# Kernel optimization log

Measured on AMD Instinct MI355X. Metric: run time of the kernel, lower is better.

## Reference

```python
import jax, jax.numpy as jnp
import numpy as np
from jax import lax

D_MODEL = 1024
D_STATE = 16
D_CONV = 4
EXPAND = 2
D_INNER = EXPAND * D_MODEL  # 2048
DT_RANK = (D_MODEL + 15) // 16  # 64 (ceil(d_model/16), mamba default)
BATCH = 2
SEQLEN = 1024


def setup_inputs() -> dict:
    key = jax.random.key(0)
    ks = jax.random.split(key, 12)
    s = lambda k, shape, sc=0.02: jax.random.normal(k, shape, jnp.float32) * sc
    # A init: S4D-real, A_log = log(1..d_state) tiled over channels
    A_log = jnp.log(jnp.tile(jnp.arange(1, D_STATE + 1, dtype=jnp.float32), (D_INNER, 1)))
    # dt bias init so softplus(dt_bias) ~ 0.01
    dt_bias = jnp.log(jnp.expm1(jnp.full((D_INNER,), 0.01, jnp.float32)))
    return {
        "x": jax.random.normal(ks[0], (BATCH, SEQLEN, D_MODEL), jnp.float32),
        "in_proj_w": s(ks[1], (2 * D_INNER, D_MODEL)),
        "conv_w": s(ks[2], (D_INNER, 1, D_CONV), 0.1),
        "conv_b": s(ks[3], (D_INNER,), 0.1),
        "x_proj_w": s(ks[4], (DT_RANK + 2 * D_STATE, D_INNER)),
        "dt_proj_w": s(ks[5], (D_INNER, DT_RANK), 0.1),
        "dt_proj_b": dt_bias,
        "A_log": A_log,
        "D": jnp.ones((D_INNER,), jnp.float32),
        "out_proj_w": s(ks[6], (D_MODEL, D_INNER)),
        "ln1_g": jnp.ones((D_MODEL,), jnp.float32),
        "ln1_b": jnp.zeros((D_MODEL,), jnp.float32),
        "ln2_g": jnp.ones((D_MODEL,), jnp.float32),
        "ln2_b": jnp.zeros((D_MODEL,), jnp.float32),
        "ffn_w1": s(ks[7], (4 * D_MODEL, D_MODEL)),
        "ffn_b1": jnp.zeros((4 * D_MODEL,), jnp.float32),
        "ffn_w2": s(ks[8], (D_MODEL, 4 * D_MODEL)),
        "ffn_b2": jnp.zeros((D_MODEL,), jnp.float32),
    }


def _layernorm(x, g, b, eps=1e-5):
    mu = jnp.mean(x, axis=-1, keepdims=True)
    var = jnp.mean(jnp.square(x - mu), axis=-1, keepdims=True)
    return (x - mu) * lax.rsqrt(var + eps) * g + b


def _mamba(x, in_proj_w, conv_w, conv_b, x_proj_w, dt_proj_w, dt_proj_b,
           A_log, D, out_proj_w):
    Bsz, L, _ = x.shape
    xz = x @ in_proj_w.T                       # [B, L, 2*d_inner]
    xi, z = jnp.split(xz, 2, axis=-1)          # each [B, L, d_inner]
    # causal depthwise conv1d over time
    xc = xi.transpose(0, 2, 1)                 # [B, d_inner, L]
    xc = lax.conv_general_dilated(
        xc, conv_w, window_strides=(1,), padding=[(D_CONV - 1, 0)],
        feature_group_count=D_INNER,
        dimension_numbers=("NCH", "OIH", "NCH"))
    xc = xc + conv_b[None, :, None]
    xc = jax.nn.silu(xc).transpose(0, 2, 1)    # [B, L, d_inner]
    # input-dependent SSM params
    x_dbl = xc @ x_proj_w.T                    # [B, L, dt_rank + 2*d_state]
    dt, Bmat, Cmat = jnp.split(x_dbl, [DT_RANK, DT_RANK + D_STATE], axis=-1)
    dt = jax.nn.softplus(dt @ dt_proj_w.T + dt_proj_b)   # [B, L, d_inner]
    A = -jnp.exp(A_log)                        # [d_inner, d_state]
    dA = jnp.exp(dt[..., None] * A)                       # [B, L, d_inner, d_state]
    dBx = dt[..., None] * Bmat[:, :, None, :] * xc[..., None]  # [B, L, d_inner, d_state]
    # selective scan over time
    def step(h, inp):
        dA_t, dBx_t, C_t = inp
        h = dA_t * h + dBx_t                   # [B, d_inner, d_state]
        y = jnp.einsum("bdn,bn->bd", h, C_t)
        return h, y
    h0 = jnp.zeros((Bsz, D_INNER, D_STATE), x.dtype)
    _, ys = lax.scan(step, h0,
                     (dA.transpose(1, 0, 2, 3),
                      dBx.transpose(1, 0, 2, 3),
                      Cmat.transpose(1, 0, 2)))
    y = ys.transpose(1, 0, 2)                  # [B, L, d_inner]
    y = y + D * xc
    y = y * jax.nn.silu(z)
    return y @ out_proj_w.T                    # [B, L, d_model]


def reference(x, in_proj_w, conv_w, conv_b, x_proj_w, dt_proj_w, dt_proj_b,
              A_log, D, out_proj_w, ln1_g, ln1_b, ln2_g, ln2_b,
              ffn_w1, ffn_b1, ffn_w2, ffn_b2):
    # x = x + Mamba(LN1(x))
    x = x + _mamba(_layernorm(x, ln1_g, ln1_b), in_proj_w, conv_w, conv_b,
                   x_proj_w, dt_proj_w, dt_proj_b, A_log, D, out_proj_w)
    # x = x + FFN(LN2(x))  (dropout inactive in eval)
    h = _layernorm(x, ln2_g, ln2_b)
    f = jax.nn.relu(h @ ffn_w1.T + ffn_b1) @ ffn_w2.T + ffn_b2
    return x + f
```

## Files before the change

kernel.cpp:

```cpp
#include <hip/hip_runtime.h>
#include <hip/hip_bf16.h>

#define T_TOK 2048
#define LSEQ  1024
#define DM    1024
#define DI    2048
#define LDW2  72

using bf16 = __hip_bfloat16;
typedef __attribute__((ext_vector_type(8))) short short8;
typedef __attribute__((ext_vector_type(4))) short short4b;
typedef __attribute__((ext_vector_type(4))) float floatx4;

__device__ inline float to_f(float v) { return v; }
__device__ inline float to_f(bf16 v) { return __bfloat162float(v); }
__device__ inline bf16  f2bf(float v) { return __float2bfloat16(v); }
__device__ inline float bf2f(short s) { return __bfloat162float(__builtin_bit_cast(bf16, s)); }

__device__ inline short8 ld8(const bf16* p) { return *(const short8*)p; }
__device__ inline short8 ld8(const float* p) {
    floatx4 f0 = *(const floatx4*)p;
    floatx4 f1 = *(const floatx4*)(p + 4);
    short8 r;
#pragma unroll
    for (int i = 0; i < 4; ++i) {
        r[i]     = __builtin_bit_cast(short, __float2bfloat16(f0[i]));
        r[i + 4] = __builtin_bit_cast(short, __float2bfloat16(f1[i]));
    }
    return r;
}

__device__ __forceinline__ void gload16(const void* g, void* l) {
    __builtin_amdgcn_global_load_lds(
        (const __attribute__((address_space(1))) unsigned int*)g,
        (__attribute__((address_space(3))) unsigned int*)l, 16, 0, 0);
}

__device__ __forceinline__ int swz32(int row, int col) {
    return row * 32 + (col ^ (((row >> 1) & 3) << 3));
}

template<int EPI, int KS>
__device__ __forceinline__ void gemm_core(
    const bf16* __restrict__ A, int lda,
    const bf16* __restrict__ W, int K,
    float* __restrict__ outF, bf16* __restrict__ outB, int ldc,
    const float* __restrict__ bias, size_t zstr)
{
    __shared__ __align__(16) bf16 sA[2][128 * 32];
    __shared__ __align__(16) bf16 sW[2][128 * 32];
    const int tid  = threadIdx.x;
    const int lane = tid & 63, wid = tid >> 6;

    const int nwg = gridDim.x * gridDim.y * gridDim.z;
    const int lin = blockIdx.x + gridDim.x * (blockIdx.y + gridDim.y * blockIdx.z);
    const int sid = (lin & 7) * (nwg >> 3) + (lin >> 3);
    const int bx  = sid % gridDim.x;
    const int byz = sid / gridDim.x;
    const int by  = byz % gridDim.y;
    const int bz  = byz / gridDim.y;

    const int m0 = bx * 128, n0 = by * 128;
    const int wm = (wid >> 1) * 64, wn = (wid & 1) * 64;
    const int lr = lane & 15, lh = lane >> 4;

    const int r0  = tid >> 2;
    const int gc0 = ((tid & 3) * 8) ^ (((r0 >> 1) & 3) << 3);

    const int kBeg = bz * (K / KS);
    const int kEnd = kBeg + K / KS;

    const bf16* aR0 = A + (size_t)(m0 + r0)      * lda + gc0;
    const bf16* aR1 = A + (size_t)(m0 + r0 + 64) * lda + gc0;
    const bf16* wR0 = W + (size_t)(n0 + r0)      * K   + gc0;
    const bf16* wR1 = W + (size_t)(n0 + r0 + 64) * K   + gc0;

    floatx4 acc[4][4];
#pragma unroll
    for (int i = 0; i < 4; ++i)
#pragma unroll
        for (int j = 0; j < 4; ++j) acc[i][j] = (floatx4){0.f, 0.f, 0.f, 0.f};

#define STAGE(B, KK) do {                                       \
        gload16(aR0 + (KK), &sA[B][wid * 512]);                 \
        gload16(aR1 + (KK), &sA[B][2048 + wid * 512]);          \
        gload16(wR0 + (KK), &sW[B][wid * 512]);                 \
        gload16(wR1 + (KK), &sW[B][2048 + wid * 512]);          \
    } while (0)

#define COMPUTE(B) do {                                                        \
        short8 af[4], wf[4];                                                   \
        _Pragma("unroll")                                                      \
        for (int i = 0; i < 4; ++i)                                            \
            af[i] = *(const short8*)(&sA[B][swz32(wm + i * 16 + lr, lh * 8)]); \
        _Pragma("unroll")                                                      \
        for (int j = 0; j < 4; ++j)                                            \
            wf[j] = *(const short8*)(&sW[B][swz32(wn + j * 16 + lr, lh * 8)]); \
        _Pragma("unroll")                                                      \
        for (int i = 0; i < 4; ++i)                                            \
            _Pragma("unroll")                                                  \
            for (int j = 0; j < 4; ++j)                                        \
                acc[i][j] = __builtin_amdgcn_mfma_f32_16x16x32_bf16(           \
                    af[i], wf[j], acc[i][j], 0, 0, 0);                         \
    } while (0)

#define PHASE_SYNC() do {                                       \
        __builtin_amdgcn_sched_barrier(0);                      \
        asm volatile("s_waitcnt vmcnt(0)" ::: "memory");        \
        __builtin_amdgcn_s_barrier();                           \
        __builtin_amdgcn_sched_barrier(0);                      \
    } while (0)

    STAGE(0, kBeg);
    PHASE_SYNC();

    for (int k0 = kBeg; k0 < kEnd; k0 += 64) {
        STAGE(1, k0 + 32);
        COMPUTE(0);
        PHASE_SYNC();
        int kn = (k0 + 64 < kEnd) ? k0 + 64 : kBeg;
        STAGE(0, kn);
        COMPUTE(1);
        PHASE_SYNC();
    }
#undef STAGE
#undef COMPUTE
#undef PHASE_SYNC

#pragma unroll
    for (int i = 0; i < 4; ++i) {
#pragma unroll
        for (int j = 0; j < 4; ++j) {
#pragma unroll
            for (int r = 0; r < 4; ++r) {
                int row = m0 + wm + i * 16 + lh * 4 + r;
                int col = n0 + wn + j * 16 + lr;
                size_t off = (size_t)row * ldc + col;
                float c = acc[i][j][r];
                if (EPI == 0) {
                    outB[off] = f2bf(c);
                } else if (EPI == 2) {
                    float v = c + bias[col];
                    outB[off] = f2bf((v > 15.f) ? v : log1pf(__expf(v)));
                } else if (EPI == 4) {
                    float v = c + bias[col];
                    outB[off] = f2bf(v > 0.f ? v : 0.f);
                } else if (EPI == 7) {
                    outF[off + (size_t)bz * zstr] = c;
                } else if (EPI == 8) {
                    outB[off + (size_t)bz * zstr] = f2bf(c);
                }
            }
        }
    }
}

__launch_bounds__(256, 3)
__global__ void g_inproj(const bf16* __restrict__ A, const bf16* __restrict__ W,
                         bf16* __restrict__ outB)
{ gemm_core<0, 1>(A, DM, W, DM, nullptr, outB, 4096, nullptr, 0); }

__launch_bounds__(256, 3)
__global__ void g_xproj(const bf16* __restrict__ A, const bf16* __restrict__ W,
                        float* __restrict__ outF)
{ gemm_core<7, 16>(A, DI, W, DI, outF, nullptr, 128, nullptr, (size_t)T_TOK * 128); }

__launch_bounds__(256, 3)
__global__ void g_outproj(const bf16* __restrict__ A, const bf16* __restrict__ W,
                          bf16* __restrict__ outB)
{ gemm_core<8, 4>(A, DI, W, DI, nullptr, outB, DM, nullptr, (size_t)T_TOK * DM); }

__launch_bounds__(256, 3)
__global__ void g_ffn1(const bf16* __restrict__ A, const bf16* __restrict__ W,
                       bf16* __restrict__ outB, const float* __restrict__ bias)
{ gemm_core<4, 1>(A, DM, W, DM, nullptr, outB, 4096, bias, 0); }

__launch_bounds__(256, 3)
__global__ void g_ffn2_4(const bf16* __restrict__ A, const bf16* __restrict__ W,
                         bf16* __restrict__ outB)
{ gemm_core<8, 4>(A, 4096, W, 4096, nullptr, outB, DM, nullptr, (size_t)T_TOK * DM); }

__launch_bounds__(256, 3)
__global__ void g_ffn2_2(const bf16* __restrict__ A, const bf16* __restrict__ W,
                         bf16* __restrict__ outB)
{ gemm_core<8, 2>(A, 4096, W, 4096, nullptr, outB, DM, nullptr, (size_t)T_TOK * DM); }

__launch_bounds__(256)
__global__ void cvtw(const float* __restrict__ src, bf16* __restrict__ dst)
{
    size_t i = ((size_t)blockIdx.x * 256 + threadIdx.x) * 8;
    *(short8*)(dst + i) = ld8(src + i);
}

__launch_bounds__(256)
__global__ void cvtw5(const float* __restrict__ s0, bf16* __restrict__ d0,
                      const float* __restrict__ s1, bf16* __restrict__ d1,
                      const float* __restrict__ s2, bf16* __restrict__ d2,
                      const float* __restrict__ s3, bf16* __restrict__ d3,
                      const float* __restrict__ s4, bf16* __restrict__ d4)
{
    constexpr size_t N0 = (size_t)2 * DI * DM;
    constexpr size_t N1 = (size_t)DM * DI;
    constexpr size_t N2 = (size_t)4 * DM * DM;
    constexpr size_t N3 = (size_t)DM * 4 * DM;
    size_t i = ((size_t)blockIdx.x * 256 + threadIdx.x) * 8;
    if (i < N0) { *(short8*)(d0 + i) = ld8(s0 + i); return; }
    i -= N0;
    if (i < N1) { *(short8*)(d1 + i) = ld8(s1 + i); return; }
    i -= N1;
    if (i < N2) { *(short8*)(d2 + i) = ld8(s2 + i); return; }
    i -= N2;
    if (i < N3) { *(short8*)(d3 + i) = ld8(s3 + i); return; }
    i -= N3;
    int row = (int)(i >> 11);
    if (row < 96) { *(short8*)(d4 + i) = ld8(s4 + i); }
    else { *(short8*)(d4 + i) = (short8){0,0,0,0,0,0,0,0}; }
}

__launch_bounds__(256)
__global__ void gemm_dt64(const float* __restrict__ A,
                          const float* __restrict__ W,
                          const float* __restrict__ bias,
                          bf16* __restrict__ outB)
{
    __shared__ __align__(16) bf16 sA[32 * LDW2];
    __shared__ __align__(16) bf16 sW[128 * LDW2];
    const int tid = threadIdx.x;
    const int lane = tid & 63, w = tid >> 6;
    const int m0 = blockIdx.x * 32, n0 = blockIdx.y * 128;

    {
        int ar = tid >> 3, ac = (tid & 7) * 8;
        *(short8*)(sA + ar * LDW2 + ac) = ld8(A + (size_t)(m0 + ar) * 128 + ac);
        int wr = tid >> 1, wc = (tid & 1) * 32;
        const float* wp = W + (size_t)(n0 + wr) * 64 + wc;
        *(short8*)(sW + wr * LDW2 + wc)      = ld8(wp);
        *(short8*)(sW + wr * LDW2 + wc + 8)  = ld8(wp + 8);
        *(short8*)(sW + wr * LDW2 + wc + 16) = ld8(wp + 16);
        *(short8*)(sW + wr * LDW2 + wc + 24) = ld8(wp + 24);
    }
    __syncthreads();

    const int lr = lane & 15, lh = lane >> 4;
    floatx4 acc[2][2];
#pragma unroll
    for (int i = 0; i < 2; ++i)
#pragma unroll
        for (int j = 0; j < 2; ++j) acc[i][j] = (floatx4){0.f, 0.f, 0.f, 0.f};

#pragma unroll
    for (int kk = 0; kk < 2; ++kk) {
        short8 af[2], wf[2];
#pragma unroll
        for (int i = 0; i < 2; ++i)
            af[i] = *(const short8*)(sA + (i * 16 + lr) * LDW2 + kk * 32 + lh * 8);
#pragma unroll
        for (int j = 0; j < 2; ++j)
            wf[j] = *(const short8*)(sW + (w * 32 + j * 16 + lr) * LDW2 + kk * 32 + lh * 8);
#pragma unroll
        for (int i = 0; i < 2; ++i)
#pragma unroll
            for (int j = 0; j < 2; ++j)
                acc[i][j] = __builtin_amdgcn_mfma_f32_16x16x32_bf16(af[i], wf[j], acc[i][j], 0, 0, 0);
    }

#pragma unroll
    for (int i = 0; i < 2; ++i) {
#pragma unroll
        for (int j = 0; j < 2; ++j) {
#pragma unroll
            for (int r = 0; r < 4; ++r) {
                int row = m0 + i * 16 + lh * 4 + r;
                int col = n0 + w * 32 + j * 16 + lr;
                float v = acc[i][j][r] + bias[col];
                outB[(size_t)row * DI + col] = f2bf((v > 15.f) ? v : log1pf(__expf(v)));
            }
        }
    }
}

__launch_bounds__(256)
__global__ void reduce16(const float* __restrict__ P, float* __restrict__ out)
{
    int i = blockIdx.x * 256 + threadIdx.x;
    const floatx4* P4 = (const floatx4*)P;
    floatx4 s = (floatx4){0.f, 0.f, 0.f, 0.f};
#pragma unroll
    for (int z = 0; z < 16; ++z) s += P4[(size_t)z * 65536 + i];
    ((floatx4*)out)[i] = s;
}

__launch_bounds__(256)
__global__ void red4_ln(const bf16* __restrict__ P, const float* __restrict__ x,
                        const float* __restrict__ g, const float* __restrict__ bb,
                        float* __restrict__ x2, bf16* __restrict__ h1)
{
    int t = blockIdx.x, tid = threadIdx.x;
    size_t rowoff = (size_t)t * DM + tid * 4;
    floatx4 xv = *(const floatx4*)(x + rowoff);
    float v[4];
#pragma unroll
    for (int i = 0; i < 4; ++i) v[i] = xv[i];
#pragma unroll
    for (int z = 0; z < 4; ++z) {
        short4b p = *(const short4b*)(P + (size_t)z * T_TOK * DM + rowoff);
#pragma unroll
        for (int i = 0; i < 4; ++i) v[i] += bf2f(p[i]);
    }
    *(floatx4*)(x2 + rowoff) = (floatx4){v[0], v[1], v[2], v[3]};
    float s = v[0] + v[1] + v[2] + v[3];
    float ss = v[0]*v[0] + v[1]*v[1] + v[2]*v[2] + v[3]*v[3];
#pragma unroll
    for (int o = 1; o < 64; o <<= 1) { s += __shfl_xor(s, o); ss += __shfl_xor(ss, o); }
    __shared__ float red[8];
    int lane = tid & 63, wid = tid >> 6;
    if (lane == 0) { red[wid] = s; red[wid + 4] = ss; }
    __syncthreads();
    s  = red[0] + red[1] + red[2] + red[3];
    ss = red[4] + red[5] + red[6] + red[7];
    float mu  = s * (1.f / DM);
    float var = ss * (1.f / DM) - mu * mu;
    float rs  = rsqrtf(var + 1e-5f);
    int c = tid * 4;
    short4b o4;
#pragma unroll
    for (int i = 0; i < 4; ++i)
        o4[i] = __builtin_bit_cast(short, f2bf((v[i] - mu) * rs * g[c + i] + bb[c + i]));
    *(short4b*)(h1 + rowoff) = o4;
}

template<int Z>
__launch_bounds__(256)
__global__ void red_bias_resid(const bf16* __restrict__ P, const float* __restrict__ bias,
                               const float* __restrict__ resid, float* __restrict__ out)
{
    size_t base = ((size_t)blockIdx.x * 256 + threadIdx.x) * 8;
    int c = (int)(base & (DM - 1));
    floatx4 b0 = *(const floatx4*)(bias + c);
    floatx4 b1 = *(const floatx4*)(bias + c + 4);
    floatx4 x0 = *(const floatx4*)(resid + base);
    floatx4 x1 = *(const floatx4*)(resid + base + 4);
    float s[8];
#pragma unroll
    for (int j = 0; j < 4; ++j) { s[j] = x0[j] + b0[j]; s[j + 4] = x1[j] + b1[j]; }
#pragma unroll
    for (int z = 0; z < Z; ++z) {
        short8 p = *(const short8*)(P + (size_t)z * T_TOK * DM + base);
#pragma unroll
        for (int j = 0; j < 8; ++j) s[j] += bf2f(p[j]);
    }
    *(floatx4*)(out + base)     = (floatx4){s[0], s[1], s[2], s[3]};
    *(floatx4*)(out + base + 4) = (floatx4){s[4], s[5], s[6], s[7]};
}

__launch_bounds__(256)
__global__ void ln_kernel(const float* __restrict__ x, const float* __restrict__ g,
                          const float* __restrict__ bb, bf16* __restrict__ out)
{
    int t = blockIdx.x, tid = threadIdx.x;
    const float* xr = x + (size_t)t * DM;
    float v[4], s = 0.f, ss = 0.f;
#pragma unroll
    for (int i = 0; i < 4; ++i) {
        v[i] = xr[tid + i * 256];
        s += v[i]; ss += v[i] * v[i];
    }
#pragma unroll
    for (int o = 1; o < 64; o <<= 1) { s += __shfl_xor(s, o); ss += __shfl_xor(ss, o); }
    __shared__ float red[8];
    int lane = tid & 63, wid = tid >> 6;
    if (lane == 0) { red[wid] = s; red[wid + 4] = ss; }
    __syncthreads();
    s  = red[0] + red[1] + red[2] + red[3];
    ss = red[4] + red[5] + red[6] + red[7];
    float mu  = s * (1.f / DM);
    float var = ss * (1.f / DM) - mu * mu;
    float rs  = rsqrtf(var + 1e-5f);
#pragma unroll
    for (int i = 0; i < 4; ++i) {
        int c = tid + i * 256;
        out[(size_t)t * DM + c] = f2bf((v[i] - mu) * rs * g[c] + bb[c]);
    }
}

__launch_bounds__(256)
__global__ void conv_silu(const bf16* __restrict__ xz, const float* __restrict__ cw,
                          const float* __restrict__ cb, bf16* __restrict__ xcb)
{
    int idx = (blockIdx.x * 256 + threadIdx.x) * 8;
    int d  = idx & (DI - 1);
    int tk = idx >> 11;
    int t  = tk & (LSEQ - 1);
    const short8 zero = {0, 0, 0, 0, 0, 0, 0, 0};
    short8 x3 = ld8(xz + (size_t)tk * 4096 + d);
    short8 x2 = (t >= 1) ? ld8(xz + (size_t)(tk - 1) * 4096 + d) : zero;
    short8 x1 = (t >= 2) ? ld8(xz + (size_t)(tk - 2) * 4096 + d) : zero;
    short8 x0 = (t >= 3) ? ld8(xz + (size_t)(tk - 3) * 4096 + d) : zero;
    short8 r;
#pragma unroll
    for (int j = 0; j < 8; ++j) {
        floatx4 wv = *(const floatx4*)(cw + (size_t)(d + j) * 4);
        float acc = cb[d + j]
                  + wv[0] * bf2f(x0[j]) + wv[1] * bf2f(x1[j])
                  + wv[2] * bf2f(x2[j]) + wv[3] * bf2f(x3[j]);
        float s = acc / (1.f + __expf(-acc));
        r[j] = __builtin_bit_cast(short, f2bf(s));
    }
    *(short8*)(xcb + idx) = r;
}

__launch_bounds__(256)
__global__ void padw_kernel(const float* __restrict__ w, bf16* __restrict__ wp)
{
    int idx = blockIdx.x * 256 + threadIdx.x;
    int row = idx >> 11;
    wp[idx] = (row < 96) ? f2bf(w[idx]) : f2bf(0.f);
}

template<int NCH_>
__launch_bounds__(256)
__global__ void scan_part1(const bf16* __restrict__ dt, const bf16* __restrict__ xc,
                           const float* __restrict__ xdbl, const float* __restrict__ A_log,
                           float* __restrict__ Ssum, float* __restrict__ hend)
{
    constexpr int CLEN_ = LSEQ / NCH_;
    constexpr int LOGN  = (NCH_ == 64) ? 6 : 5;
    int G = blockIdx.x * 256 + threadIdx.x;
    int half = G & 1;
    int d = (G >> 1) & (DI - 1);
    int c = (G >> 12) & (NCH_ - 1);
    int b = G >> (12 + LOGN);
    int n0 = half * 8;

    floatx4 al0 = *(const floatx4*)(A_log + d * 16 + n0);
    floatx4 al1 = *(const floatx4*)(A_log + d * 16 + n0 + 4);
    float a[8];
#pragma unroll
    for (int j = 0; j < 4; ++j) { a[j] = -__expf(al0[j]); a[j + 4] = -__expf(al1[j]); }

    const bf16*  dt_p = dt   + (size_t)b * LSEQ * DI + d;
    const bf16*  xc_p = xc   + (size_t)b * LSEQ * DI + d;
    const float* xb_p = xdbl + (size_t)b * LSEQ * 128 + 64 + n0;

    float h[8];
#pragma unroll
    for (int j = 0; j < 8; ++j) h[j] = 0.f;
    float S = 0.f;

    const int t0 = c * CLEN_;
#pragma unroll 4
    for (int t = t0; t < t0 + CLEN_; ++t) {
        float dtv = to_f(dt_p[(size_t)t * DI]);
        float xv  = to_f(xc_p[(size_t)t * DI]);
        floatx4 B0 = *(const floatx4*)(xb_p + (size_t)t * 128);
        floatx4 B1 = *(const floatx4*)(xb_p + (size_t)t * 128 + 4);
        S += dtv;
        float dx = dtv * xv;
#pragma unroll
        for (int j = 0; j < 4; ++j) {
            h[j]     = fmaf(__expf(dtv * a[j]),     h[j],     dx * B0[j]);
            h[j + 4] = fmaf(__expf(dtv * a[j + 4]), h[j + 4], dx * B1[j]);
        }
    }

    size_t cid = (size_t)(b * NCH_ + c) * DI + d;
    if (half == 0) Ssum[cid] = S;
    float* he = hend + cid * 16 + n0;
    *(floatx4*)he       = (floatx4){h[0], h[1], h[2], h[3]};
    *(floatx4*)(he + 4) = (floatx4){h[4], h[5], h[6], h[7]};
}

template<int NCH_>
__launch_bounds__(256)
__global__ void scan_prefix(const float* __restrict__ A_log, const float* __restrict__ Ssum,
                            float* __restrict__ hend)
{
    int tid = blockIdx.x * 256 + threadIdx.x;
    int n = tid & 15;
    int d = (tid >> 4) & (DI - 1);
    int b = tid >> 15;
    float a = -__expf(A_log[d * 16 + n]);

    size_t row = (size_t)b * NCH_ * DI + d;
    float Sc = Ssum[row];
    float E  = hend[row * 16 + n];
    float h = 0.f;
    for (int c = 0; c < NCH_; ++c) {
        size_t nrow = row + DI;
        float Sn = 0.f, En = 0.f;
        if (c + 1 < NCH_) { Sn = Ssum[nrow]; En = hend[nrow * 16 + n]; }
        float P = __expf(a * Sc);
        hend[row * 16 + n] = h;
        h  = fmaf(P, h, E);
        Sc = Sn; E = En; row = nrow;
    }
}

template<int NCH_>
__launch_bounds__(256)
__global__ void scan_part2(const bf16* __restrict__ dt, const bf16* __restrict__ xc,
                           const float* __restrict__ xdbl, const bf16* __restrict__ xz,
                           const float* __restrict__ hinit, const float* __restrict__ A_log,
                           const float* __restrict__ Dp, bf16* __restrict__ Y)
{
    constexpr int CLEN_ = LSEQ / NCH_;
    constexpr int LOGN  = (NCH_ == 64) ? 6 : 5;
    int G = blockIdx.x * 256 + threadIdx.x;
    int half = G & 1;
    int d = (G >> 1) & (DI - 1);
    int c = (G >> 12) & (NCH_ - 1);
    int b = G >> (12 + LOGN);
    int n0 = half * 8;

    floatx4 al0 = *(const floatx4*)(A_log + d * 16 + n0);
    floatx4 al1 = *(const floatx4*)(A_log + d * 16 + n0 + 4);
    float a[8];
#pragma unroll
    for (int j = 0; j < 4; ++j) { a[j] = -__expf(al0[j]); a[j + 4] = -__expf(al1[j]); }
    float Dd = Dp[d];

    size_t cid = (size_t)(b * NCH_ + c) * DI + d;
    const float* hi = hinit + cid * 16 + n0;
    floatx4 h0 = *(const floatx4*)hi;
    floatx4 h1 = *(const floatx4*)(hi + 4);
    float h[8] = {h0[0], h0[1], h0[2], h0[3], h1[0], h1[1], h1[2], h1[3]};

    const bf16*  dt_p = dt   + (size_t)b * LSEQ * DI + d;
    const bf16*  xc_p = xc   + (size_t)b * LSEQ * DI + d;
    const float* xb_p = xdbl + (size_t)b * LSEQ * 128 + 64 + n0;
    const float* xcc_p= xdbl + (size_t)b * LSEQ * 128 + 80 + n0;
    const bf16*  z_p  = xz   + (size_t)b * LSEQ * 4096 + DI + d;
    bf16* y_p = Y + (size_t)b * LSEQ * DI + d;

    const int t0 = c * CLEN_;
#pragma unroll 4
    for (int t = t0; t < t0 + CLEN_; ++t) {
        float dtv = to_f(dt_p[(size_t)t * DI]);
        float xv  = to_f(xc_p[(size_t)t * DI]);
        float zv  = to_f(z_p[(size_t)t * 4096]);
        floatx4 B0 = *(const floatx4*)(xb_p  + (size_t)t * 128);
        floatx4 B1 = *(const floatx4*)(xb_p  + (size_t)t * 128 + 4);
        floatx4 C0 = *(const floatx4*)(xcc_p + (size_t)t * 128);
        floatx4 C1 = *(const floatx4*)(xcc_p + (size_t)t * 128 + 4);
        float dx = dtv * xv;
        float p = 0.f;
#pragma unroll
        for (int j = 0; j < 4; ++j) {
            h[j]     = fmaf(__expf(dtv * a[j]),     h[j],     dx * B0[j]);
            p = fmaf(h[j], C0[j], p);
            h[j + 4] = fmaf(__expf(dtv * a[j + 4]), h[j + 4], dx * B1[j]);
            p = fmaf(h[j + 4], C1[j], p);
        }
        p += __shfl_xor(p, 1);
        if (half == 0) {
            float pp = p + Dd * xv;
            float sz = zv / (1.f + __expf(-zv));
            y_p[(size_t)t * DI] = f2bf(pp * sz);
        }
    }
}

extern "C" void kernel_launch(void* const* d_in, const int* in_sizes, int n_in,
                              void* d_out, int out_size, void* d_ws, size_t ws_size,
                              hipStream_t stream)
{
    const float* x       = (const float*)d_in[0];
    const float* in_proj = (const float*)d_in[1];
    const float* conv_w  = (const float*)d_in[2];
    const float* conv_b  = (const float*)d_in[3];
    const float* x_proj  = (const float*)d_in[4];
    const float* dt_w    = (const float*)d_in[5];
    const float* dt_b    = (const float*)d_in[6];
    const float* A_log   = (const float*)d_in[7];
    const float* Dp      = (const float*)d_in[8];
    const float* out_w   = (const float*)d_in[9];
    const float* ln1g    = (const float*)d_in[10];
    const float* ln1b    = (const float*)d_in[11];
    const float* ln2g    = (const float*)d_in[12];
    const float* ln2b    = (const float*)d_in[13];
    const float* fw1     = (const float*)d_in[14];
    const float* fb1     = (const float*)d_in[15];
    const float* fw2     = (const float*)d_in[16];
    const float* fb2     = (const float*)d_in[17];
    float* out = (float*)d_out;

    char* w = (char*)d_ws;
    bf16*  h1   = (bf16*)(w);
    bf16*  xz   = (bf16*)(w + (4u  << 20));
    bf16*  xc   = (bf16*)(w + (20u << 20));
    float* xdf  = (float*)(w + (28u << 20));
    bf16*  dtb  = (bf16*)(w + (29u << 20));
    float* Pp   = (float*)(w + (29u << 20));
    float* hend = (float*)(w + (37u << 20));
    float* x2   = (float*)(w + (37u << 20));
    bf16*  Wpad = (bf16*)(w + (45u << 20));
    float* Ssum = (float*)(w);
    bf16*  Pout = (bf16*)(w + (4u  << 20));
    bf16*  Yb = xc;
    bf16*  f1 = xz;

    const bool roomy = ws_size >= ((size_t)74 << 20);

    if (roomy) {
        bf16* ipB  = (bf16*)(w + (46u << 20));
        bf16* owB  = (bf16*)(w + (54u << 20));
        bf16* fw1B = (bf16*)(w + (58u << 20));
        bf16* fw2B = (bf16*)(w + (66u << 20));
        bf16* Pf   = (bf16*)(w + (20u << 20));

        cvtw5<<<dim3(7296), dim3(256), 0, stream>>>(in_proj, ipB, out_w, owB,
                                                    fw1, fw1B, fw2, fw2B, x_proj, Wpad);
        ln_kernel<<<dim3(T_TOK), dim3(256), 0, stream>>>(x, ln1g, ln1b, h1);
        g_inproj<<<dim3(16, 32), dim3(256), 0, stream>>>(h1, ipB, xz);
        conv_silu<<<dim3(T_TOK * DI / 8 / 256), dim3(256), 0, stream>>>(xz, conv_w, conv_b, xc);
        g_xproj<<<dim3(16, 1, 16), dim3(256), 0, stream>>>(xc, Wpad, Pp);
        reduce16<<<dim3(256), dim3(256), 0, stream>>>(Pp, xdf);
        gemm_dt64<<<dim3(64, 16), dim3(256), 0, stream>>>(xdf, dt_w, dt_b, dtb);
        scan_part1<64><<<dim3(2048), dim3(256), 0, stream>>>(dtb, xc, xdf, A_log, Ssum, hend);
        scan_prefix<64><<<dim3(256), dim3(256), 0, stream>>>(A_log, Ssum, hend);
        scan_part2<64><<<dim3(2048), dim3(256), 0, stream>>>(dtb, xc, xdf, xz, hend, A_log, Dp, Yb);
        g_outproj<<<dim3(16, 8, 4), dim3(256), 0, stream>>>(Yb, owB, Pout);
        red4_ln<<<dim3(T_TOK), dim3(256), 0, stream>>>(Pout, x, ln2g, ln2b, x2, h1);
        g_ffn1<<<dim3(16, 32), dim3(256), 0, stream>>>(h1, fw1B, f1, fb1);
        g_ffn2_4<<<dim3(16, 8, 4), dim3(256), 0, stream>>>(f1, fw2B, Pf);
        red_bias_resid<4><<<dim3(1024), dim3(256), 0, stream>>>(Pf, fb2, x2, out);
    } else {
        bf16* ipB  = (bf16*)(w + (20u << 20));
        bf16* owB  = (bf16*)(w);
        bf16* fw1B = (bf16*)(w + (29u << 20));
        bf16* fw2B = (bf16*)(w + (20u << 20));
        bf16* Pf   = (bf16*)(w + (28u << 20));

        cvtw<<<dim3(2048), dim3(256), 0, stream>>>(in_proj, ipB);
        ln_kernel<<<dim3(T_TOK), dim3(256), 0, stream>>>(x, ln1g, ln1b, h1);
        g_inproj<<<dim3(16, 32), dim3(256), 0, stream>>>(h1, ipB, xz);
        conv_silu<<<dim3(T_TOK * DI / 8 / 256), dim3(256), 0, stream>>>(xz, conv_w, conv_b, xc);
        padw_kernel<<<dim3(128 * 2048 / 256), dim3(256), 0, stream>>>(x_proj, Wpad);
        g_xproj<<<dim3(16, 1, 16), dim3(256), 0, stream>>>(xc, Wpad, Pp);
        reduce16<<<dim3(256), dim3(256), 0, stream>>>(Pp, xdf);
        gemm_dt64<<<dim3(64, 16), dim3(256), 0, stream>>>(xdf, dt_w, dt_b, dtb);
        scan_part1<32><<<dim3(1024), dim3(256), 0, stream>>>(dtb, xc, xdf, A_log, Ssum, hend);
        scan_prefix<32><<<dim3(256), dim3(256), 0, stream>>>(A_log, Ssum, hend);
        cvtw<<<dim3(1024), dim3(256), 0, stream>>>(out_w, owB);
        scan_part2<32><<<dim3(1024), dim3(256), 0, stream>>>(dtb, xc, xdf, xz, hend, A_log, Dp, Yb);
        g_outproj<<<dim3(16, 8, 4), dim3(256), 0, stream>>>(Yb, owB, Pout);
        cvtw<<<dim3(2048), dim3(256), 0, stream>>>(fw1, fw1B);
        red4_ln<<<dim3(T_TOK), dim3(256), 0, stream>>>(Pout, x, ln2g, ln2b, x2, h1);
        g_ffn1<<<dim3(16, 32), dim3(256), 0, stream>>>(h1, fw1B, f1, fb1);
        cvtw<<<dim3(2048), dim3(256), 0, stream>>>(fw2, fw2B);
        g_ffn2_2<<<dim3(16, 8, 2), dim3(256), 0, stream>>>(f1, fw2B, Pf);
        red_bias_resid<2><<<dim3(1024), dim3(256), 0, stream>>>(Pf, fb2, x2, out);
    }
}
```

Measured before the change: 377.2 us.

## Use 512-thread GEMM blocks with single-buffered LDS and smaller per-wave tiles

```diff
diff --git a/kernel.cpp b/kernel.cpp
--- a/kernel.cpp
+++ b/kernel.cpp
@@ -47,8 +47,8 @@
     float* __restrict__ outF, bf16* __restrict__ outB, int ldc,
     const float* __restrict__ bias, size_t zstr)
 {
-    __shared__ __align__(16) bf16 sA[2][128 * 32];
-    __shared__ __align__(16) bf16 sW[2][128 * 32];
+    __shared__ __align__(16) bf16 sA[128 * 32];
+    __shared__ __align__(16) bf16 sW[128 * 32];
     const int tid  = threadIdx.x;
     const int lane = tid & 63, wid = tid >> 6;
 
@@ -61,7 +61,8 @@
     const int bz  = byz / gridDim.y;
 
     const int m0 = bx * 128, n0 = by * 128;
-    const int wm = (wid >> 1) * 64, wn = (wid & 1) * 64;
+    const int wm = (wid >> 2) * 64;
+    const int wn = (wid & 3) * 32;
     const int lr = lane & 15, lh = lane >> 4;
 
     const int r0  = tid >> 2;
@@ -70,67 +71,43 @@
     const int kBeg = bz * (K / KS);
     const int kEnd = kBeg + K / KS;
 
-    const bf16* aR0 = A + (size_t)(m0 + r0)      * lda + gc0;
-    const bf16* aR1 = A + (size_t)(m0 + r0 + 64) * lda + gc0;
-    const bf16* wR0 = W + (size_t)(n0 + r0)      * K   + gc0;
-    const bf16* wR1 = W + (size_t)(n0 + r0 + 64) * K   + gc0;
-
-    floatx4 acc[4][4];
+    const bf16* Ag = A + (size_t)(m0 + r0) * lda + kBeg + gc0;
+    const bf16* Wg = W + (size_t)(n0 + r0) * K   + kBeg + gc0;
+
+    bf16* sAd = sA + wid * 512;
+    bf16* sWd = sW + wid * 512;
+
+    floatx4 acc[4][2];
 #pragma unroll
     for (int i = 0; i < 4; ++i)
 #pragma unroll
-        for (int j = 0; j < 4; ++j) acc[i][j] = (floatx4){0.f, 0.f, 0.f, 0.f};
-
-#define STAGE(B, KK) do {                                       \
-        gload16(aR0 + (KK), &sA[B][wid * 512]);                 \
-        gload16(aR1 + (KK), &sA[B][2048 + wid * 512]);          \
-        gload16(wR0 + (KK), &sW[B][wid * 512]);                 \
-        gload16(wR1 + (KK), &sW[B][2048 + wid * 512]);          \
-    } while (0)
-
-#define COMPUTE(B) do {                                                        \
-        short8 af[4], wf[4];                                                   \
-        _Pragma("unroll")                                                      \
-        for (int i = 0; i < 4; ++i)                                            \
-            af[i] = *(const short8*)(&sA[B][swz32(wm + i * 16 + lr, lh * 8)]); \
-        _Pragma("unroll")                                                      \
-        for (int j = 0; j < 4; ++j)                                            \
-            wf[j] = *(const short8*)(&sW[B][swz32(wn + j * 16 + lr, lh * 8)]); \
-        _Pragma("unroll")                                                      \
-        for (int i = 0; i < 4; ++i)                                            \
-            _Pragma("unroll")                                                  \
-            for (int j = 0; j < 4; ++j)                                        \
-                acc[i][j] = __builtin_amdgcn_mfma_f32_16x16x32_bf16(           \
-                    af[i], wf[j], acc[i][j], 0, 0, 0);                         \
-    } while (0)
-
-#define PHASE_SYNC() do {                                       \
-        __builtin_amdgcn_sched_barrier(0);                      \
-        asm volatile("s_waitcnt vmcnt(0)" ::: "memory");        \
-        __builtin_amdgcn_s_barrier();                           \
-        __builtin_amdgcn_sched_barrier(0);                      \
-    } while (0)
-
-    STAGE(0, kBeg);
-    PHASE_SYNC();
-
-    for (int k0 = kBeg; k0 < kEnd; k0 += 64) {
-        STAGE(1, k0 + 32);
-        COMPUTE(0);
-        PHASE_SYNC();
-        int kn = (k0 + 64 < kEnd) ? k0 + 64 : kBeg;
-        STAGE(0, kn);
-        COMPUTE(1);
-        PHASE_SYNC();
-    }
-#undef STAGE
-#undef COMPUTE
-#undef PHASE_SYNC
+        for (int j = 0; j < 2; ++j) acc[i][j] = (floatx4){0.f, 0.f, 0.f, 0.f};
+
+    for (int k0 = kBeg; k0 < kEnd; k0 += 32) {
+        __syncthreads();
+        gload16(Ag, sAd);
+        gload16(Wg, sWd);
+        Ag += 32; Wg += 32;
+        __syncthreads();
+
+        short8 af[4], wf[2];
+#pragma unroll
+        for (int i = 0; i < 4; ++i)
+            af[i] = *(const short8*)(sA + swz32(wm + i * 16 + lr, lh * 8));
+#pragma unroll
+        for (int j = 0; j < 2; ++j)
+            wf[j] = *(const short8*)(sW + swz32(wn + j * 16 + lr, lh * 8));
+#pragma unroll
+        for (int i = 0; i < 4; ++i)
+#pragma unroll
+            for (int j = 0; j < 2; ++j)
+                acc[i][j] = __builtin_amdgcn_mfma_f32_16x16x32_bf16(af[i], wf[j], acc[i][j], 0, 0, 0);
+    }
 
 #pragma unroll
     for (int i = 0; i < 4; ++i) {
 #pragma unroll
-        for (int j = 0; j < 4; ++j) {
+        for (int j = 0; j < 2; ++j) {
 #pragma unroll
             for (int r = 0; r < 4; ++r) {
                 int row = m0 + wm + i * 16 + lh * 4 + r;
@@ -155,32 +132,32 @@
     }
 }
 
-__launch_bounds__(256, 3)
+__launch_bounds__(512, 4)
 __global__ void g_inproj(const bf16* __restrict__ A, const bf16* __restrict__ W,
                          bf16* __restrict__ outB)
 { gemm_core<0, 1>(A, DM, W, DM, nullptr, outB, 4096, nullptr, 0); }
 
-__launch_bounds__(256, 3)
+__launch_bounds__(512, 4)
 __global__ void g_xproj(const bf16* __restrict__ A, const bf16* __restrict__ W,
                         float* __restrict__ outF)
 { gemm_core<7, 16>(A, DI, W, DI, outF, nullptr, 128, nullptr, (size_t)T_TOK * 128); }
 
-__launch_bounds__(256, 3)
+__launch_bounds__(512, 4)
 __global__ void g_outproj(const bf16* __restrict__ A, const bf16* __restrict__ W,
                           bf16* __restrict__ outB)
 { gemm_core<8, 4>(A, DI, W, DI, nullptr, outB, DM, nullptr, (size_t)T_TOK * DM); }
 
-__launch_bounds__(256, 3)
+__launch_bounds__(512, 4)
 __global__ void g_ffn1(const bf16* __restrict__ A, const bf16* __restrict__ W,
                        bf16* __restrict__ outB, const float* __restrict__ bias)
 { gemm_core<4, 1>(A, DM, W, DM, nullptr, outB, 4096, bias, 0); }
 
-__launch_bounds__(256, 3)
+__launch_bounds__(512, 4)
 __global__ void g_ffn2_4(const bf16* __restrict__ A, const bf16* __restrict__ W,
                          bf16* __restrict__ outB)
 { gemm_core<8, 4>(A, 4096, W, 4096, nullptr, outB, DM, nullptr, (size_t)T_TOK * DM); }
 
-__launch_bounds__(256, 3)
+__launch_bounds__(512, 4)
 __global__ void g_ffn2_2(const bf16* __restrict__ A, const bf16* __restrict__ W,
                          bf16* __restrict__ outB)
 { gemm_core<8, 2>(A, 4096, W, 4096, nullptr, outB, DM, nullptr, (size_t)T_TOK * DM); }
@@ -611,18 +588,18 @@
         cvtw5<<<dim3(7296), dim3(256), 0, stream>>>(in_proj, ipB, out_w, owB,
                                                     fw1, fw1B, fw2, fw2B, x_proj, Wpad);
         ln_kernel<<<dim3(T_TOK), dim3(256), 0, stream>>>(x, ln1g, ln1b, h1);
-        g_inproj<<<dim3(16, 32), dim3(256), 0, stream>>>(h1, ipB, xz);
+        g_inproj<<<dim3(16, 32), dim3(512), 0, stream>>>(h1, ipB, xz);
         conv_silu<<<dim3(T_TOK * DI / 8 / 256), dim3(256), 0, stream>>>(xz, conv_w, conv_b, xc);
-        g_xproj<<<dim3(16, 1, 16), dim3(256), 0, stream>>>(xc, Wpad, Pp);
+        g_xproj<<<dim3(16, 1, 16), dim3(512), 0, stream>>>(xc, Wpad, Pp);
         reduce16<<<dim3(256), dim3(256), 0, stream>>>(Pp, xdf);
         gemm_dt64<<<dim3(64, 16), dim3(256), 0, stream>>>(xdf, dt_w, dt_b, dtb);
         scan_part1<64><<<dim3(2048), dim3(256), 0, stream>>>(dtb, xc, xdf, A_log, Ssum, hend);
         scan_prefix<64><<<dim3(256), dim3(256), 0, stream>>>(A_log, Ssum, hend);
         scan_part2<64><<<dim3(2048), dim3(256), 0, stream>>>(dtb, xc, xdf, xz, hend, A_log, Dp, Yb);
-        g_outproj<<<dim3(16, 8, 4), dim3(256), 0, stream>>>(Yb, owB, Pout);
+        g_outproj<<<dim3(16, 8, 4), dim3(512), 0, stream>>>(Yb, owB, Pout);
         red4_ln<<<dim3(T_TOK), dim3(256), 0, stream>>>(Pout, x, ln2g, ln2b, x2, h1);
-        g_ffn1<<<dim3(16, 32), dim3(256), 0, stream>>>(h1, fw1B, f1, fb1);
-        g_ffn2_4<<<dim3(16, 8, 4), dim3(256), 0, stream>>>(f1, fw2B, Pf);
+        g_ffn1<<<dim3(16, 32), dim3(512), 0, stream>>>(h1, fw1B, f1, fb1);
+        g_ffn2_4<<<dim3(16, 8, 4), dim3(512), 0, stream>>>(f1, fw2B, Pf);
         red_bias_resid<4><<<dim3(1024), dim3(256), 0, stream>>>(Pf, fb2, x2, out);
     } else {
         bf16* ipB  = (bf16*)(w + (20u << 20));
@@ -633,22 +610,22 @@
 
         cvtw<<<dim3(2048), dim3(256), 0, stream>>>(in_proj, ipB);
         ln_kernel<<<dim3(T_TOK), dim3(256), 0, stream>>>(x, ln1g, ln1b, h1);
-        g_inproj<<<dim3(16, 32), dim3(256), 0, stream>>>(h1, ipB, xz);
+        g_inproj<<<dim3(16, 32), dim3(512), 0, stream>>>(h1, ipB, xz);
         conv_silu<<<dim3(T_TOK * DI / 8 / 256), dim3(256), 0, stream>>>(xz, conv_w, conv_b, xc);
         padw_kernel<<<dim3(128 * 2048 / 256), dim3(256), 0, stream>>>(x_proj, Wpad);
-        g_xproj<<<dim3(16, 1, 16), dim3(256), 0, stream>>>(xc, Wpad, Pp);
+        g_xproj<<<dim3(16, 1, 16), dim3(512), 0, stream>>>(xc, Wpad, Pp);
         reduce16<<<dim3(256), dim3(256), 0, stream>>>(Pp, xdf);
         gemm_dt64<<<dim3(64, 16), dim3(256), 0, stream>>>(xdf, dt_w, dt_b, dtb);
         scan_part1<32><<<dim3(1024), dim3(256), 0, stream>>>(dtb, xc, xdf, A_log, Ssum, hend);
         scan_prefix<32><<<dim3(256), dim3(256), 0, stream>>>(A_log, Ssum, hend);
         cvtw<<<dim3(1024), dim3(256), 0, stream>>>(out_w, owB);
         scan_part2<32><<<dim3(1024), dim3(256), 0, stream>>>(dtb, xc, xdf, xz, hend, A_log, Dp, Yb);
-        g_outproj<<<dim3(16, 8, 4), dim3(256), 0, stream>>>(Yb, owB, Pout);
+        g_outproj<<<dim3(16, 8, 4), dim3(512), 0, stream>>>(Yb, owB, Pout);
         cvtw<<<dim3(2048), dim3(256), 0, stream>>>(fw1, fw1B);
         red4_ln<<<dim3(T_TOK), dim3(256), 0, stream>>>(Pout, x, ln2g, ln2b, x2, h1);
-        g_ffn1<<<dim3(16, 32), dim3(256), 0, stream>>>(h1, fw1B, f1, fb1);
+        g_ffn1<<<dim3(16, 32), dim3(512), 0, stream>>>(h1, fw1B, f1, fb1);
         cvtw<<<dim3(2048), dim3(256), 0, stream>>>(fw2, fw2B);
-        g_ffn2_2<<<dim3(16, 8, 2), dim3(256), 0, stream>>>(f1, fw2B, Pf);
+        g_ffn2_2<<<dim3(16, 8, 2), dim3(512), 0, stream>>>(f1, fw2B, Pf);
         red_bias_resid<2><<<dim3(1024), dim3(256), 0, stream>>>(Pf, fb2, x2, out);
     }
 }
```

After: 352.7 us. -6.5%, faster.
